# Performance work log

Measured on AMD Instinct MI355X. Metric: run time of the kernel, lower is better.

Reference implementation:

```python
import jax, jax.numpy as jnp
import numpy as np

V_NT, V_RULE, E, H = 200, 500, 1024, 1024  # H == E so cat([nt_emb, prod_emb]) == E + H
B, T, L_NL, L_ENV = 32, 128, 512, 512


def setup_inputs() -> dict:
    key = jax.random.key(0)
    ks = jax.random.split(key, 20)
    s = 0.02
    return {
        'init_prod': jax.random.randint(ks[0], (B,), 0, V_RULE),
        'nt_ids': jax.random.randint(ks[1], (T, B), 0, V_NT),
        'h0': jax.random.normal(ks[2], (B, H), jnp.float32),
        'c0': jax.random.normal(ks[3], (B, H), jnp.float32),
        'nl_encoding': jax.random.normal(ks[4], (B, L_NL, H), jnp.float32),
        'env_encoding': jax.random.normal(ks[5], (B, L_ENV, H), jnp.float32),
        'nt_emb': jax.random.normal(ks[6], (V_NT, E), jnp.float32) * s,
        'rule_emb': jax.random.normal(ks[7], (V_RULE, E), jnp.float32) * s,
        'W_ih': jax.random.normal(ks[8], (4 * H, E + H), jnp.float32) * s,
        'W_hh': jax.random.normal(ks[9], (4 * H, H), jnp.float32) * s,
        'b_ih': jnp.zeros((4 * H,), jnp.float32),
        'b_hh': jnp.zeros((4 * H,), jnp.float32),
        'Wz': jax.random.normal(ks[10], (H, 2 * H), jnp.float32) * s,
        'bz': jnp.zeros((H,), jnp.float32),
        'We': jax.random.normal(ks[11], (H, 2 * H), jnp.float32) * s,
        'be': jnp.zeros((H,), jnp.float32),
        'Wc': jax.random.normal(ks[12], (H, 3 * H), jnp.float32) * s,
        'bc': jnp.zeros((H,), jnp.float32),
    }


def _attention(query, context, W, b):
    # query: (B, H), context: (B, L, H)
    scores = jnp.einsum('bh,blh->bl', query, context)          # bmm(output, context^T)
    attn = jax.nn.softmax(scores, axis=-1)                     # softmax over input_len
    mix = jnp.einsum('bl,blh->bh', attn, context)              # bmm(attn, context)
    out = jnp.tanh(jnp.concatenate([mix, query], axis=-1) @ W.T + b)
    return out, attn


def reference(init_prod, nt_ids, h0, c0, nl_encoding, env_encoding,
              nt_emb, rule_emb, W_ih, W_hh, b_ih, b_hh,
              Wz, bz, We, be, Wc, bc):
    last_prod = rule_emb[init_prod]  # (B, E); never updated in the source loop

    def step(carry, nt_t):
        h, c = carry
        x = jnp.concatenate([nt_emb[nt_t], last_prod], axis=-1)  # (B, E+H)
        gates = x @ W_ih.T + b_ih + h @ W_hh.T + b_hh             # (B, 4H)
        i, f, g, o = jnp.split(gates, 4, axis=-1)                 # torch gate order i,f,g,o
        i = jax.nn.sigmoid(i); f = jax.nn.sigmoid(f)
        g = jnp.tanh(g); o = jax.nn.sigmoid(o)
        c_new = f * c + i * g
        h_new = o * jnp.tanh(c_new)
        st = h_new                                                # (B, H)
        zt, _ = _attention(st, nl_encoding, Wz, bz)               # nl cross-attention
        et, _ = _attention(zt, env_encoding, We, be)              # env cross-attention
        ct = jnp.tanh(jnp.concatenate([st, zt, et], axis=-1) @ Wc.T + bc)
        return (h_new, c_new), ct

    _, cts = jax.lax.scan(step, (h0, c0), nt_ids)  # cts: (T, B, H)
    return cts
```

## Files before the change

### kernel.cpp

```cpp
#include <hip/hip_runtime.h>
#include <hip/hip_bf16.h>

typedef _Float16 f16;
typedef __attribute__((ext_vector_type(8))) _Float16 f16x8;
typedef __attribute__((ext_vector_type(4))) float f32x4;
typedef __attribute__((ext_vector_type(4))) unsigned int u32x4;
typedef __attribute__((ext_vector_type(2))) int i32x2;

#define TT 128

__device__ __forceinline__ float sigmoidf_(float x) { return 1.0f / (1.0f + __expf(-x)); }

__global__ __launch_bounds__(256) void k_prep(
    const float* __restrict__ W_ih, const float* __restrict__ W_hh,
    const float* __restrict__ Wz, const float* __restrict__ We,
    const float* __restrict__ Wc, const float* __restrict__ nt_emb,
    const float* __restrict__ rule_emb, const int* __restrict__ init_prod,
    const float* __restrict__ h0,
    f16* __restrict__ Wih_h, f16* __restrict__ Whh_h,
    f16* __restrict__ Wz_h, f16* __restrict__ We_h, f16* __restrict__ Wc_h,
    f16* __restrict__ nte_h, f16* __restrict__ prod_h,
    f16* __restrict__ st, int* __restrict__ bar)
{
  const long nWih = 2097152, nWhh = 1048576, nWz = 524288, nWe = 524288,
             nWc = 786432, nNte = 51200, nGat = 32768, nH0 = 32768, nZ = 512;
  const long T0 = nWih, T1 = T0 + nWhh, T2 = T1 + nWz, T3 = T2 + nWe,
             T4 = T3 + nWc, T5 = T4 + nNte, T6 = T5 + nGat, T7 = T6 + nH0,
             T8 = T7 + nZ;
  const long stride = (long)gridDim.x * 256;
  for (long i = (long)blockIdx.x * 256 + threadIdx.x; i < T8; i += stride) {
    if (i < T5) {
      const float* src; f16* dst; long j;
      if (i < T0)      { src = W_ih;   dst = Wih_h; j = i; }
      else if (i < T1) { src = W_hh;   dst = Whh_h; j = i - T0; }
      else if (i < T2) { src = Wz;     dst = Wz_h;  j = i - T1; }
      else if (i < T3) { src = We;     dst = We_h;  j = i - T2; }
      else if (i < T4) { src = Wc;     dst = Wc_h;  j = i - T3; }
      else             { src = nt_emb; dst = nte_h; j = i - T4; }
      float4 v = ((const float4*)src)[j];
      dst[j*4+0] = (f16)v.x; dst[j*4+1] = (f16)v.y;
      dst[j*4+2] = (f16)v.z; dst[j*4+3] = (f16)v.w;
    } else if (i < T6) {
      long j = i - T5; int b = (int)(j >> 10), k = (int)(j & 1023);
      prod_h[j] = (f16)rule_emb[(long)init_prod[b] * 1024 + k];
    } else if (i < T7) {
      long j = i - T6; int b = (int)(j >> 10), k = (int)(j & 1023);
      st[(long)(k >> 3) * 256 + b * 8 + (k & 7)] = (f16)h0[j];
    } else {
      bar[i - T7] = 0;
    }
  }
}

__global__ __launch_bounds__(256) void k_transpose(const float* __restrict__ in,
                                                   f16* __restrict__ outT,
                                                   f16* __restrict__ outN) {
  __shared__ float tile[32][33];
  const int b  = blockIdx.z;
  const int l0 = blockIdx.x * 32, h0 = blockIdx.y * 32;
  in   += (long)b * 512 * 1024;
  outT += (long)b * 1024 * 512;
  outN += (long)b * 512 * 1024;
  const int c = threadIdx.x & 31, r = threadIdx.x >> 5;
#pragma unroll
  for (int p = 0; p < 4; ++p) {
    float v = in[(long)(l0 + r + p*8) * 1024 + h0 + c];
    tile[r + p*8][c] = v;
    outN[(long)(l0 + r + p*8) * 1024 + h0 + c] = (f16)v;
  }
  __syncthreads();
#pragma unroll
  for (int p = 0; p < 4; ++p)
    outT[(long)(h0 + r + p*8) * 512 + l0 + c] = (f16)tile[c][r + p*8];
}

__global__ __launch_bounds__(256) void k_gemm(
    const f16* __restrict__ A, long lda, long sA,
    const f16* __restrict__ B, long ldb, long sB,
    float* __restrict__ outF, long ldF, long sF, long sSl,
    f16* __restrict__ outH, long ldH, long sH,
    f16* __restrict__ outH2, long ldH2, long sH2,
    f16* __restrict__ out2, long ld2, long s2,
    const float* __restrict__ bias1, const float* __restrict__ bias2,
    int M, int N, int K, int act, int bmod, int zdiv, int ilv)
{
  __shared__ __align__(16) f16 As[128][40];
  __shared__ __align__(16) f16 Bs[128][40];
  const int tid = threadIdx.x;
  const int w = tid >> 6, lane = tid & 63;
  const int wm = (w & 1) * 64, wn = (w >> 1) * 64;
  const int lr = lane >> 4, lc = lane & 15;
  const long m0 = (long)blockIdx.x * 128;
  const long n0 = (long)blockIdx.y * 128;
  int z = blockIdx.z, batch = z, slice = 0, Ks = K;
  if (zdiv > 1) { batch = z / zdiv; slice = z - batch * zdiv; Ks = K / zdiv; }
  const long kbeg = (long)slice * Ks;
  A += (long)batch * sA;
  B += (long)batch * sB;

  const int rr = tid >> 2, sg = (tid & 3) * 8;
  const int nIt = Ks / 32;

  uint4 pa[2], pb[2];
  {
    long k = kbeg;
    long kb = bmod ? (k & (bmod - 1)) : k;
#pragma unroll
    for (int p = 0; p < 2; ++p) {
      int row = p * 64 + rr;
      uint4 va = {0,0,0,0}, vb = {0,0,0,0};
      if (m0 + row < M) va = *(const uint4*)(A + (m0 + row) * lda + k + sg);
      if (n0 + row < N) vb = *(const uint4*)(B + (n0 + row) * ldb + kb + sg);
      pa[p] = va; pb[p] = vb;
    }
  }

  f32x4 acc[4][4];
#pragma unroll
  for (int i = 0; i < 4; ++i)
#pragma unroll
    for (int j = 0; j < 4; ++j) { f32x4 zz = {0.f,0.f,0.f,0.f}; acc[i][j] = zz; }

  for (int it = 0; it < nIt; ++it) {
#pragma unroll
    for (int p = 0; p < 2; ++p) {
      *(uint4*)&As[p * 64 + rr][sg] = pa[p];
      *(uint4*)&Bs[p * 64 + rr][sg] = pb[p];
    }
    __syncthreads();
    if (it + 1 < nIt) {
      long k = kbeg + (long)(it + 1) * 32;
      long kb = bmod ? (k & (bmod - 1)) : k;
#pragma unroll
      for (int p = 0; p < 2; ++p) {
        int row = p * 64 + rr;
        uint4 va = {0,0,0,0}, vb = {0,0,0,0};
        if (m0 + row < M) va = *(const uint4*)(A + (m0 + row) * lda + k + sg);
        if (n0 + row < N) vb = *(const uint4*)(B + (n0 + row) * ldb + kb + sg);
        pa[p] = va; pb[p] = vb;
      }
    }
    f16x8 af[4], bf[4];
#pragma unroll
    for (int i = 0; i < 4; ++i) af[i] = *(const f16x8*)&As[wm + i*16 + lc][lr * 8];
#pragma unroll
    for (int j = 0; j < 4; ++j) bf[j] = *(const f16x8*)&Bs[wn + j*16 + lc][lr * 8];
#pragma unroll
    for (int i = 0; i < 4; ++i)
#pragma unroll
      for (int j = 0; j < 4; ++j)
        acc[i][j] = __builtin_amdgcn_mfma_f32_16x16x32_f16(af[i], bf[j], acc[i][j], 0, 0, 0);
    __syncthreads();
  }

  if (outF)  outF  += (long)batch * sF + (long)slice * sSl;
  if (outH)  outH  += (long)batch * sH;
  if (outH2) outH2 += (long)batch * sH2;
  if (out2)  out2  += (long)batch * s2;
#pragma unroll
  for (int i = 0; i < 4; ++i)
#pragma unroll
    for (int j = 0; j < 4; ++j)
#pragma unroll
      for (int r = 0; r < 4; ++r) {
        long row = m0 + wm + i * 16 + lr * 4 + r;
        long col = n0 + wn + j * 16 + lc;
        if (row < M && col < N) {
          float v = acc[i][j][r];
          if (bias1) v += bias1[col];
          if (bias2) v += bias2[col];
          if (act)   v = tanhf(v);
          if (outF) {
            long fc = ilv ? ((col & 1023) * 4 + (col >> 10)) : col;
            outF[row * ldF + fc] = v;
          }
          if (outH)  outH[row * ldH + col] = (f16)v;
          if (outH2) outH2[row * ldH2 + col] = (f16)v;
          if (out2) {
            f16 hi = (f16)v;
            out2[row * ld2 + col]        = hi;
            out2[row * ld2 + 1024 + col] = (f16)(v - (float)hi);
          }
        }
      }
}

__global__ __launch_bounds__(256) void k_lstm_all(
    const f16* __restrict__ Whh,
    const float* __restrict__ nt_table,
    const float* __restrict__ prod_gates,
    const int* __restrict__ nt_ids,
    const float* __restrict__ c0,
    f16* __restrict__ st,
    f16* __restrict__ q2,
    f16* __restrict__ X,
    f16* __restrict__ Y1,
    int* __restrict__ flags,
    const float* __restrict__ nl,
    f16* __restrict__ ctxT, f16* __restrict__ ctxN)
{
  __shared__ __align__(16) f16 whh_s[32][1032];
  __shared__ float partial[2][4][32][34];
  __shared__ float tile[32][33];
  const int tid = threadIdx.x;
  const int bx = blockIdx.x;

  if (bx >= 128) {
    const int me = bx - 128;
    const int c = tid & 31, r = tid >> 5;
    for (int idx = me; idx < 16384; idx += 128) {
      int b = idx >> 9, rr2 = idx & 511;
      int l0 = (rr2 & 15) * 32, h0v = (rr2 >> 4) * 32;
      const float* inb = nl + (long)b * 512 * 1024;
      f16* oTb = ctxT + (long)b * 1024 * 512;
      f16* oNb = ctxN + (long)b * 512 * 1024;
#pragma unroll
      for (int p = 0; p < 4; ++p) {
        float v = inb[(long)(l0 + r + p*8) * 1024 + h0v + c];
        tile[r + p*8][c] = v;
        oNb[(long)(l0 + r + p*8) * 1024 + h0v + c] = (f16)v;
      }
      __syncthreads();
#pragma unroll
      for (int p = 0; p < 4; ++p)
        oTb[(long)(h0v + r + p*8) * 512 + l0 + c] = (f16)tile[c][r + p*8];
      __syncthreads();
    }
    return;
  }

  const int w = tid >> 6, lane = tid & 63;
  const int lr = lane >> 4, lc = lane & 15;
  const int j0 = bx * 8;

  for (int i = tid; i < 32 * 128; i += 256) {
    int r = i >> 7, c8 = i & 127;
    int g = r >> 3, jj = r & 7;
    *(uint4*)&whh_s[r][c8 * 8] =
        *(const uint4*)(Whh + ((long)g * 1024 + j0 + jj) * 1024 + c8 * 8);
  }
  const int b_own = tid >> 3, jj_own = tid & 7;
  const int j_own = j0 + jj_own;
  float c_reg = c0[(long)b_own * 1024 + j_own];
  float4 pg4 = *(const float4*)(prod_gates + (long)b_own * 4096 + j_own * 4);
  int nid0 = nt_ids[b_own];
  float4 nt4 = *(const float4*)(nt_table + (long)nid0 * 4096 + j_own * 4);
  __syncthreads();

  f16x8 B0[8], B1[8];
#pragma unroll
  for (int kt = 0; kt < 8; ++kt) {
    int k = w * 256 + kt * 32 + lr * 8;
    B0[kt] = *(const f16x8*)&whh_s[lc][k];
    B1[kt] = *(const f16x8*)&whh_s[16 + lc][k];
  }

  const f16* pA = st + (long)(w * 32 + lr) * 256 + lc * 8;
  const int* fp = flags + w * 128 + lane * 2;

  for (int t = 0; t < TT; ++t) {
    if (t > 0) {
      int done = 0;
      while (true) {
        if (!done) {
          i32x2 ff;
          asm volatile("global_load_dwordx2 %0, %1, off sc0 sc1\n\t"
                       "s_waitcnt vmcnt(0)"
                       : "=&v"(ff) : "v"(fp) : "memory");
          done = (ff.x >= t) & (ff.y >= t);
        }
        if (__all(done)) break;
        __builtin_amdgcn_s_sleep(1);
      }
    }

    u32x4 A0[8], A1[8];
    {
      const f16* pt = pA + (long)t * 32768;
#pragma unroll
      for (int q = 0; q < 4; ++q) {
        asm volatile(
          "global_load_dwordx4 %0, %4, off sc0 sc1\n\t"
          "global_load_dwordx4 %1, %4, off offset:256 sc0 sc1\n\t"
          "global_load_dwordx4 %2, %4, off offset:2048 sc0 sc1\n\t"
          "global_load_dwordx4 %3, %4, off offset:2304 sc0 sc1"
          : "=&v"(A0[2*q]), "=&v"(A1[2*q]), "=&v"(A0[2*q+1]), "=&v"(A1[2*q+1])
          : "v"(pt + (long)q * 2048) : "memory");
      }
      asm volatile("s_waitcnt vmcnt(0)" ::: "memory");
      __builtin_amdgcn_sched_barrier(0);
    }

    float4 nt4n = nt4;
    if (t + 1 < TT) {
      int nidn = nt_ids[(t + 1) * 32 + b_own];
      nt4n = *(const float4*)(nt_table + (long)nidn * 4096 + j_own * 4);
    }

    f32x4 acc[2][2];
#pragma unroll
    for (int i = 0; i < 2; ++i)
#pragma unroll
      for (int j = 0; j < 2; ++j) { f32x4 zz = {0.f,0.f,0.f,0.f}; acc[i][j] = zz; }
#pragma unroll
    for (int kt = 0; kt < 8; ++kt) {
      f16x8 a0v = __builtin_bit_cast(f16x8, A0[kt]);
      f16x8 a1v = __builtin_bit_cast(f16x8, A1[kt]);
      acc[0][0] = __builtin_amdgcn_mfma_f32_16x16x32_f16(a0v, B0[kt], acc[0][0], 0, 0, 0);
      acc[0][1] = __builtin_amdgcn_mfma_f32_16x16x32_f16(a0v, B1[kt], acc[0][1], 0, 0, 0);
      acc[1][0] = __builtin_amdgcn_mfma_f32_16x16x32_f16(a1v, B0[kt], acc[1][0], 0, 0, 0);
      acc[1][1] = __builtin_amdgcn_mfma_f32_16x16x32_f16(a1v, B1[kt], acc[1][1], 0, 0, 0);
    }
    float (*pp)[32][34] = partial[t & 1];
#pragma unroll
    for (int mi = 0; mi < 2; ++mi)
#pragma unroll
      for (int ni = 0; ni < 2; ++ni)
#pragma unroll
        for (int r = 0; r < 4; ++r)
          pp[w][ni * 16 + lc][mi * 16 + lr * 4 + r] = acc[mi][ni][r];
    __syncthreads();

    float g4[4];
#pragma unroll
    for (int g = 0; g < 4; ++g) {
      int rrow = g * 8 + jj_own;
      g4[g] = pp[0][rrow][b_own] + pp[1][rrow][b_own] +
              pp[2][rrow][b_own] + pp[3][rrow][b_own];
    }
    float ii = sigmoidf_(g4[0] + nt4.x + pg4.x);
    float ff = sigmoidf_(g4[1] + nt4.y + pg4.y);
    float gg = tanhf(g4[2] + nt4.z + pg4.z);
    float oo = sigmoidf_(g4[3] + nt4.w + pg4.w);
    c_reg = ff * c_reg + ii * gg;
    float hn = oo * tanhf(c_reg);
    f16 hi = (f16)hn;

    if (t + 1 < TT) {
      union { f16 h; unsigned short u; } cv; cv.h = hi;
      unsigned me2 = cv.u;
      unsigned d  = me2 | ((unsigned)__shfl_down((int)me2, 1) << 16);
      unsigned d2 = (unsigned)__shfl_down((int)d, 2);
      unsigned e0 = (unsigned)__shfl_down((int)d, 4);
      unsigned e1 = (unsigned)__shfl_down((int)d2, 4);
      if (jj_own == 0) {
        u32x4 pay; pay.x = d; pay.y = d2; pay.z = e0; pay.w = e1;
        f16* pst = st + (long)(t + 1) * 32768 + bx * 256 + b_own * 8;
        asm volatile("global_store_dwordx4 %0, %1, off sc0 sc1"
                     :: "v"(pst), "v"(pay) : "memory");
      }
      asm volatile("s_waitcnt vmcnt(0)" ::: "memory");
      if (lane == 0) {
        int* myf = flags + bx * 4 + w;
        int fv = t + 1;
        asm volatile("global_store_dword %0, %1, off sc0 sc1"
                     :: "v"(myf), "v"(fv) : "memory");
      }
    }

    long row = (long)b_own * 128 + t;
    q2[row * 2048 + j_own]        = hi;
    q2[row * 2048 + 1024 + j_own] = (f16)(hn - (float)hi);
    X[row * 3072 + j_own]         = hi;
    Y1[row * 2048 + 1024 + j_own] = hi;

    nt4 = nt4n;
  }
}

__global__ __launch_bounds__(256) void k_softmax4(const float* __restrict__ p,
                                                  long pstride,
                                                  f16* __restrict__ out) {
  long row = blockIdx.x;
  const float* p0 = p + row * 512;
  out += row * 512;
  const int tid = threadIdx.x, w = tid >> 6, lane = tid & 63;
  float vx = 0.f, vy = 0.f;
#pragma unroll
  for (int s = 0; s < 4; ++s) {
    float2 a = ((const float2*)(p0 + s * pstride))[tid];
    vx += a.x; vy += a.y;
  }
  float m = fmaxf(vx, vy);
#pragma unroll
  for (int off = 32; off; off >>= 1) m = fmaxf(m, __shfl_xor(m, off));
  __shared__ float red[8];
  if (lane == 0) red[w] = m;
  __syncthreads();
  m = fmaxf(fmaxf(red[0], red[1]), fmaxf(red[2], red[3]));
  float e0 = __expf(vx - m), e1 = __expf(vy - m);
  float s2 = e0 + e1;
#pragma unroll
  for (int off = 32; off; off >>= 1) s2 += __shfl_xor(s2, off);
  if (lane == 0) red[4 + w] = s2;
  __syncthreads();
  s2 = red[4] + red[5] + red[6] + red[7];
  float inv = 1.0f / s2;
  out[tid * 2]     = (f16)(e0 * inv);
  out[tid * 2 + 1] = (f16)(e1 * inv);
}

extern "C" void kernel_launch(void* const* d_in, const int* in_sizes, int n_in,
                              void* d_out, int out_size, void* d_ws, size_t ws_size,
                              hipStream_t stream)
{
  const int*   init_prod = (const int*)d_in[0];
  const int*   nt_ids    = (const int*)d_in[1];
  const float* h0   = (const float*)d_in[2];
  const float* c0   = (const float*)d_in[3];
  const float* nl   = (const float*)d_in[4];
  const float* env  = (const float*)d_in[5];
  const float* nt_emb   = (const float*)d_in[6];
  const float* rule_emb = (const float*)d_in[7];
  const float* W_ih = (const float*)d_in[8];
  const float* W_hh = (const float*)d_in[9];
  const float* b_ih = (const float*)d_in[10];
  const float* b_hh = (const float*)d_in[11];
  const float* Wz   = (const float*)d_in[12];
  const float* bz   = (const float*)d_in[13];
  const float* We   = (const float*)d_in[14];
  const float* be   = (const float*)d_in[15];
  const float* Wc   = (const float*)d_in[16];
  const float* bc   = (const float*)d_in[17];
  float* out = (float*)d_out;
  (void)in_sizes; (void)n_in; (void)out_size; (void)ws_size;

  size_t off = 0;
  auto carve = [&](size_t bytes) {
    char* p = (char*)d_ws + off;
    off += (bytes + 255) & ~(size_t)255;
    return (void*)p;
  };
  f16*   Whh_h   = (f16*)carve(4096L * 1024 * 2);
  f16*   Wz_h    = (f16*)carve(1024L * 2048 * 2);
  f16*   We_h    = (f16*)carve(1024L * 2048 * 2);
  f16*   Wc_h    = (f16*)carve(1024L * 3072 * 2);
  f16*   nte_h   = (f16*)carve(200L * 1024 * 2);
  f16*   prod_h  = (f16*)carve(32L * 1024 * 2);
  float* nt_table   = (float*)carve(200L * 4096 * 4);
  float* prod_gates = (float*)carve(32L * 4096 * 4);
  f16*   st_hi   = (f16*)carve(129L * 128 * 32 * 8 * 2);
  f16*   q2      = (f16*)carve(4096L * 2048 * 2);
  f16*   X       = (f16*)carve(4096L * 3072 * 2);
  f16*   Y1      = (f16*)carve(4096L * 2048 * 2);
  f16*   Y2      = (f16*)carve(4096L * 2048 * 2);
  f16*   ctx_h   = (f16*)carve(32L * 512 * 1024 * 2);
  f16*   ctxT    = (f16*)carve(32L * 1024 * 512 * 2);
  float* scoresP = (float*)carve(4L * 32 * 128 * 512 * 4);
  f16*   attn    = (f16*)carve(4096L * 512 * 2);
  int*   bar     = (int*)carve(2048);
  f16*   Wih_h   = (f16*)X;

  k_prep<<<dim3(8192), dim3(256), 0, stream>>>(
      W_ih, W_hh, Wz, We, Wc, nt_emb, rule_emb, init_prod, h0,
      Wih_h, Whh_h, Wz_h, We_h, Wc_h, nte_h, prod_h, st_hi, bar);

  auto gemm = [&](const f16* A, long lda, long sA,
                  const f16* B, long ldb, long sB,
                  float* oF, long ldF, long sF, long sSl,
                  f16* oH, long ldH, long sH,
                  f16* oH2, long ldH2, long sH2,
                  f16* o2, long ld2, long s2,
                  const float* b1, const float* b2,
                  int M, int N, int K, int act, int bmod, int zdiv, int ilv,
                  int batch) {
    dim3 grid((unsigned)((M + 127) / 128), (unsigned)((N + 127) / 128),
              (unsigned)(batch * zdiv));
    k_gemm<<<grid, dim3(256), 0, stream>>>(A, lda, sA, B, ldb, sB,
                                           oF, ldF, sF, sSl, oH, ldH, sH,
                                           oH2, ldH2, sH2, o2, ld2, s2,
                                           b1, b2, M, N, K, act, bmod, zdiv, ilv);
  };
  const long SPL = 32L * 128 * 512;

  gemm(nte_h, 1024, 0, Wih_h, 2048, 0, nt_table, 4096, 0, 0,
       nullptr,0,0, nullptr,0,0, nullptr,0,0, nullptr, nullptr,
       200, 4096, 1024, 0, 0, 1, 1, 1);
  gemm(prod_h, 1024, 0, Wih_h + 1024, 2048, 0, prod_gates, 4096, 0, 0,
       nullptr,0,0, nullptr,0,0, nullptr,0,0, b_ih, b_hh,
       32, 4096, 1024, 0, 0, 1, 1, 1);

  k_lstm_all<<<dim3(256), dim3(256), 0, stream>>>(
      Whh_h, nt_table, prod_gates, nt_ids, c0, st_hi, q2, X, Y1, bar,
      nl, ctxT, ctx_h);

  gemm(q2, 2048, 128L * 2048, ctx_h, 1024, 512L * 1024,
       scoresP, 512, 128L * 512, SPL, nullptr,0,0, nullptr,0,0, nullptr,0,0,
       nullptr, nullptr, 128, 512, 2048, 0, 1024, 4, 0, 32);
  k_softmax4<<<dim3(4096), dim3(256), 0, stream>>>(scoresP, SPL, attn);
  gemm(attn, 512, 128L * 512, ctxT, 512, 1024L * 512,
       nullptr,0,0,0, Y1, 2048, 128L * 2048, nullptr,0,0, nullptr,0,0,
       nullptr, nullptr, 128, 1024, 512, 0, 0, 1, 0, 32);
  gemm(Y1, 2048, 0, Wz_h, 2048, 0,
       nullptr,0,0,0, X + 1024, 3072, 0, Y2 + 1024, 2048, 0, q2, 2048, 0,
       bz, nullptr, 4096, 1024, 2048, 1, 0, 1, 0, 1);

  k_transpose<<<dim3(16, 32, 32), dim3(256), 0, stream>>>(env, ctxT, ctx_h);
  gemm(q2, 2048, 128L * 2048, ctx_h, 1024, 512L * 1024,
       scoresP, 512, 128L * 512, SPL, nullptr,0,0, nullptr,0,0, nullptr,0,0,
       nullptr, nullptr, 128, 512, 2048, 0, 1024, 4, 0, 32);
  k_softmax4<<<dim3(4096), dim3(256), 0, stream>>>(scoresP, SPL, attn);
  gemm(attn, 512, 128L * 512, ctxT, 512, 1024L * 512,
       nullptr,0,0,0, Y2, 2048, 128L * 2048, nullptr,0,0, nullptr,0,0,
       nullptr, nullptr, 128, 1024, 512, 0, 0, 1, 0, 32);
  gemm(Y2, 2048, 0, We_h, 2048, 0,
       nullptr,0,0,0, X + 2048, 3072, 0, nullptr,0,0, nullptr,0,0,
       be, nullptr, 4096, 1024, 2048, 1, 0, 1, 0, 1);

  gemm(X, 3072, 128L * 3072, Wc_h, 3072, 0,
       out, 32L * 1024, 1024, 0, nullptr,0,0, nullptr,0,0, nullptr,0,0,
       bc, nullptr, 128, 1024, 3072, 1, 0, 1, 0, 32);
}
```

Measured before the change: 1.100 ms.

## Merge input-gate GEMMs and fold env transpose into Wz GEMM launch

The two small input-projection GEMMs (nt_emb table and init_prod gates) become one 232-row GEMM over a zero-padded concatenated input, with bias applied only to the prod rows. The separate env-encoding transpose/convert kernel is removed and run instead by an extra z-slice of blocks inside the Wz projection GEMM. This cuts two kernel launches and lets the transpose overlap with GEMM work, at the cost of doing K=2048 over half-zero inputs and adding a branch to the GEMM kernel.

```diff
diff --git a/kernel.cpp b/kernel.cpp
--- a/kernel.cpp
+++ b/kernel.cpp
@@ -19,59 +19,38 @@
     const float* __restrict__ h0,
     f16* __restrict__ Wih_h, f16* __restrict__ Whh_h,
     f16* __restrict__ Wz_h, f16* __restrict__ We_h, f16* __restrict__ Wc_h,
-    f16* __restrict__ nte_h, f16* __restrict__ prod_h,
-    f16* __restrict__ st, int* __restrict__ bar)
+    f16* __restrict__ xcat, f16* __restrict__ st, int* __restrict__ bar)
 {
   const long nWih = 2097152, nWhh = 1048576, nWz = 524288, nWe = 524288,
-             nWc = 786432, nNte = 51200, nGat = 32768, nH0 = 32768, nZ = 512;
+             nWc = 786432;
   const long T0 = nWih, T1 = T0 + nWhh, T2 = T1 + nWz, T3 = T2 + nWe,
-             T4 = T3 + nWc, T5 = T4 + nNte, T6 = T5 + nGat, T7 = T6 + nH0,
-             T8 = T7 + nZ;
+             T4 = T3 + nWc, T5 = T4 + 475136, T6 = T5 + 32768, T7 = T6 + 512;
   const long stride = (long)gridDim.x * 256;
-  for (long i = (long)blockIdx.x * 256 + threadIdx.x; i < T8; i += stride) {
-    if (i < T5) {
+  for (long i = (long)blockIdx.x * 256 + threadIdx.x; i < T7; i += stride) {
+    if (i < T4) {
       const float* src; f16* dst; long j;
-      if (i < T0)      { src = W_ih;   dst = Wih_h; j = i; }
-      else if (i < T1) { src = W_hh;   dst = Whh_h; j = i - T0; }
-      else if (i < T2) { src = Wz;     dst = Wz_h;  j = i - T1; }
-      else if (i < T3) { src = We;     dst = We_h;  j = i - T2; }
-      else if (i < T4) { src = Wc;     dst = Wc_h;  j = i - T3; }
-      else             { src = nt_emb; dst = nte_h; j = i - T4; }
+      if (i < T0)      { src = W_ih; dst = Wih_h; j = i; }
+      else if (i < T1) { src = W_hh; dst = Whh_h; j = i - T0; }
+      else if (i < T2) { src = Wz;   dst = Wz_h;  j = i - T1; }
+      else if (i < T3) { src = We;   dst = We_h;  j = i - T2; }
+      else             { src = Wc;   dst = Wc_h;  j = i - T3; }
       float4 v = ((const float4*)src)[j];
       dst[j*4+0] = (f16)v.x; dst[j*4+1] = (f16)v.y;
       dst[j*4+2] = (f16)v.z; dst[j*4+3] = (f16)v.w;
+    } else if (i < T5) {
+      long j = i - T4; int row = (int)(j >> 11), col = (int)(j & 2047);
+      float v = 0.f;
+      if (row < 200) { if (col < 1024) v = nt_emb[(long)row * 1024 + col]; }
+      else if (col >= 1024)
+        v = rule_emb[(long)init_prod[row - 200] * 1024 + (col - 1024)];
+      xcat[j] = (f16)v;
     } else if (i < T6) {
       long j = i - T5; int b = (int)(j >> 10), k = (int)(j & 1023);
-      prod_h[j] = (f16)rule_emb[(long)init_prod[b] * 1024 + k];
-    } else if (i < T7) {
-      long j = i - T6; int b = (int)(j >> 10), k = (int)(j & 1023);
       st[(long)(k >> 3) * 256 + b * 8 + (k & 7)] = (f16)h0[j];
     } else {
-      bar[i - T7] = 0;
-    }
-  }
-}
-
-__global__ __launch_bounds__(256) void k_transpose(const float* __restrict__ in,
-                                                   f16* __restrict__ outT,
-                                                   f16* __restrict__ outN) {
-  __shared__ float tile[32][33];
-  const int b  = blockIdx.z;
-  const int l0 = blockIdx.x * 32, h0 = blockIdx.y * 32;
-  in   += (long)b * 512 * 1024;
-  outT += (long)b * 1024 * 512;
-  outN += (long)b * 512 * 1024;
-  const int c = threadIdx.x & 31, r = threadIdx.x >> 5;
-#pragma unroll
-  for (int p = 0; p < 4; ++p) {
-    float v = in[(long)(l0 + r + p*8) * 1024 + h0 + c];
-    tile[r + p*8][c] = v;
-    outN[(long)(l0 + r + p*8) * 1024 + h0 + c] = (f16)v;
-  }
-  __syncthreads();
-#pragma unroll
-  for (int p = 0; p < 4; ++p)
-    outT[(long)(h0 + r + p*8) * 512 + l0 + c] = (f16)tile[c][r + p*8];
+      bar[i - T6] = 0;
+    }
+  }
 }
 
 __global__ __launch_bounds__(256) void k_gemm(
@@ -82,11 +61,40 @@
     f16* __restrict__ outH2, long ldH2, long sH2,
     f16* __restrict__ out2, long ld2, long s2,
     const float* __restrict__ bias1, const float* __restrict__ bias2,
-    int M, int N, int K, int act, int bmod, int zdiv, int ilv)
+    int M, int N, int K, int act, int bmod, int zdiv, int ilv,
+    const float* __restrict__ tin, f16* __restrict__ toutT,
+    f16* __restrict__ toutN, int brow0)
 {
   __shared__ __align__(16) f16 As[128][40];
   __shared__ __align__(16) f16 Bs[128][40];
   const int tid = threadIdx.x;
+
+  if (tin && blockIdx.z == gridDim.z - 1) {
+    __shared__ float ttile[32][33];
+    const int me = blockIdx.y * gridDim.x + blockIdx.x;
+    const int nblk = gridDim.x * gridDim.y;
+    const int c = tid & 31, r = tid >> 5;
+    for (int idx = me; idx < 16384; idx += nblk) {
+      int b = idx >> 9, rr2 = idx & 511;
+      int l0 = (rr2 & 15) * 32, h0v = (rr2 >> 4) * 32;
+      const float* inb = tin + (long)b * 512 * 1024;
+      f16* oTb = toutT + (long)b * 1024 * 512;
+      f16* oNb = toutN + (long)b * 512 * 1024;
+#pragma unroll
+      for (int p = 0; p < 4; ++p) {
+        float v = inb[(long)(l0 + r + p*8) * 1024 + h0v + c];
+        ttile[r + p*8][c] = v;
+        oNb[(long)(l0 + r + p*8) * 1024 + h0v + c] = (f16)v;
+      }
+      __syncthreads();
+#pragma unroll
+      for (int p = 0; p < 4; ++p)
+        oTb[(long)(h0v + r + p*8) * 512 + l0 + c] = (f16)ttile[c][r + p*8];
+      __syncthreads();
+    }
+    return;
+  }
+
   const int w = tid >> 6, lane = tid & 63;
   const int wm = (w & 1) * 64, wn = (w >> 1) * 64;
   const int lr = lane >> 4, lc = lane & 15;
@@ -167,8 +175,10 @@
         long col = n0 + wn + j * 16 + lc;
         if (row < M && col < N) {
           float v = acc[i][j][r];
-          if (bias1) v += bias1[col];
-          if (bias2) v += bias2[col];
+          if (row >= brow0) {
+            if (bias1) v += bias1[col];
+            if (bias2) v += bias2[col];
+          }
           if (act)   v = tanhf(v);
           if (outF) {
             long fc = ilv ? ((col & 1023) * 4 + (col >> 10)) : col;
@@ -435,10 +445,8 @@
   f16*   Wz_h    = (f16*)carve(1024L * 2048 * 2);
   f16*   We_h    = (f16*)carve(1024L * 2048 * 2);
   f16*   Wc_h    = (f16*)carve(1024L * 3072 * 2);
-  f16*   nte_h   = (f16*)carve(200L * 1024 * 2);
-  f16*   prod_h  = (f16*)carve(32L * 1024 * 2);
-  float* nt_table   = (float*)carve(200L * 4096 * 4);
-  float* prod_gates = (float*)carve(32L * 4096 * 4);
+  f16*   xcat    = (f16*)carve(232L * 2048 * 2);
+  float* nt_table = (float*)carve(232L * 4096 * 4);
   f16*   st_hi   = (f16*)carve(129L * 128 * 32 * 8 * 2);
   f16*   q2      = (f16*)carve(4096L * 2048 * 2);
   f16*   X       = (f16*)carve(4096L * 3072 * 2);
@@ -453,7 +461,7 @@
 
   k_prep<<<dim3(8192), dim3(256), 0, stream>>>(
       W_ih, W_hh, Wz, We, Wc, nt_emb, rule_emb, init_prod, h0,
-      Wih_h, Whh_h, Wz_h, We_h, Wc_h, nte_h, prod_h, st_hi, bar);
+      Wih_h, Whh_h, Wz_h, We_h, Wc_h, xcat, st_hi, bar);
 
   auto gemm = [&](const f16* A, long lda, long sA,
                   const f16* B, long ldb, long sB,
@@ -463,51 +471,55 @@
                   f16* o2, long ld2, long s2,
                   const float* b1, const float* b2,
                   int M, int N, int K, int act, int bmod, int zdiv, int ilv,
-                  int batch) {
+                  int batch, const float* tin, f16* tT, f16* tN, int brow0) {
     dim3 grid((unsigned)((M + 127) / 128), (unsigned)((N + 127) / 128),
-              (unsigned)(batch * zdiv));
+              (unsigned)(batch * zdiv + (tin ? 1 : 0)));
     k_gemm<<<grid, dim3(256), 0, stream>>>(A, lda, sA, B, ldb, sB,
                                            oF, ldF, sF, sSl, oH, ldH, sH,
                                            oH2, ldH2, sH2, o2, ld2, s2,
-                                           b1, b2, M, N, K, act, bmod, zdiv, ilv);
+                                           b1, b2, M, N, K, act, bmod, zdiv,
+                                           ilv, tin, tT, tN, brow0);
   };
   const long SPL = 32L * 128 * 512;
 
-  gemm(nte_h, 1024, 0, Wih_h, 2048, 0, nt_table, 4096, 0, 0,
-       nullptr,0,0, nullptr,0,0, nullptr,0,0, nullptr, nullptr,
-       200, 4096, 1024, 0, 0, 1, 1, 1);
-  gemm(prod_h, 1024, 0, Wih_h + 1024, 2048, 0, prod_gates, 4096, 0, 0,
+  gemm(xcat, 2048, 0, Wih_h, 2048, 0, nt_table, 4096, 0, 0,
        nullptr,0,0, nullptr,0,0, nullptr,0,0, b_ih, b_hh,
-       32, 4096, 1024, 0, 0, 1, 1, 1);
+       232, 4096, 2048, 0, 0, 1, 1, 1, nullptr, nullptr, nullptr, 200);
 
   k_lstm_all<<<dim3(256), dim3(256), 0, stream>>>(
-      Whh_h, nt_table, prod_gates, nt_ids, c0, st_hi, q2, X, Y1, bar,
-      nl, ctxT, ctx_h);
+      Whh_h, nt_table, nt_table + 200L * 4096, nt_ids, c0, st_hi, q2, X, Y1,
+      bar, nl, ctxT, ctx_h);
 
   gemm(q2, 2048, 128L * 2048, ctx_h, 1024, 512L * 1024,
        scoresP, 512, 128L * 512, SPL, nullptr,0,0, nullptr,0,0, nullptr,0,0,
-       nullptr, nullptr, 128, 512, 2048, 0, 1024, 4, 0, 32);
+       nullptr, nullptr, 128, 512, 2048, 0, 1024, 4, 0, 32,
+       nullptr, nullptr, nullptr, 0);
   k_softmax4<<<dim3(4096), dim3(256), 0, stream>>>(scoresP, SPL, attn);
   gemm(attn, 512, 128L * 512, ctxT, 512, 1024L * 512,
        nullptr,0,0,0, Y1, 2048, 128L * 2048, nullptr,0,0, nullptr,0,0,
-       nullptr, nullptr, 128, 1024, 512, 0, 0, 1, 0, 32);
+       nullptr, nullptr, 128, 1024, 512, 0, 0, 1, 0, 32,
+       nullptr, nullptr, nullptr, 0);
   gemm(Y1, 2048, 0, Wz_h, 2048, 0,
        nullptr,0,0,0, X + 1024, 3072, 0, Y2 + 1024, 2048, 0, q2, 2048, 0,
-       bz, nullptr, 4096, 1024, 2048, 1, 0, 1, 0, 1);
-
-  k_transpose<<<dim3(16, 32, 32), dim3(256), 0, stream>>>(env, ctxT, ctx_h);
+       bz, nullptr, 4096, 1024, 2048, 1, 0, 1, 0, 1,
+       env, ctxT, ctx_h, 0);
+
   gemm(q2, 2048, 128L * 2048, ctx_h, 1024, 512L * 1024,
        scoresP, 512, 128L * 512, SPL, nullptr,0,0, nullptr,0,0, nullptr,0,0,
-       nullptr, nullptr, 128, 512, 2048, 0, 1024, 4, 0, 32);
+       nullptr, nullptr, 128, 512, 2048, 0, 1024, 4, 0, 32,
+       nullptr, nullptr, nullptr, 0);
   k_softmax4<<<dim3(4096), dim3(256), 0, stream>>>(scoresP, SPL, attn);
   gemm(attn, 512, 128L * 512, ctxT, 512, 1024L * 512,
        nullptr,0,0,0, Y2, 2048, 128L * 2048, nullptr,0,0, nullptr,0,0,
-       nullptr, nullptr, 128, 1024, 512, 0, 0, 1, 0, 32);
+       nullptr, nullptr, 128, 1024, 512, 0, 0, 1, 0, 32,
+       nullptr, nullptr, nullptr, 0);
   gemm(Y2, 2048, 0, We_h, 2048, 0,
        nullptr,0,0,0, X + 2048, 3072, 0, nullptr,0,0, nullptr,0,0,
-       be, nullptr, 4096, 1024, 2048, 1, 0, 1, 0, 1);
+       be, nullptr, 4096, 1024, 2048, 1, 0, 1, 0, 1,
+       nullptr, nullptr, nullptr, 0);
 
   gemm(X, 3072, 128L * 3072, Wc_h, 3072, 0,
        out, 32L * 1024, 1024, 0, nullptr,0,0, nullptr,0,0, nullptr,0,0,
-       bc, nullptr, 128, 1024, 3072, 1, 0, 1, 0, 32);
+       bc, nullptr, 128, 1024, 3072, 1, 0, 1, 0, 32,
+       nullptr, nullptr, nullptr, 0);
 }
```

Measured after the change: 1.100 ms. No clear change (+0.0%).
